# Optimization experiments

Hardware: AMD Instinct MI355X
Metric: run time of the kernel (lower is better)

Reference implementation:

```python
import jax, jax.numpy as jnp
import numpy as np

B, N, D, H, L = 1024, 500, 128, 8, 2  # batch, nb_nodes, dim_emb, nb_heads, nb_layers_decoder
CLIP = 10.0


def _mha(q, K, V, h, mask, clip):
    # q: (B,1,D) single query; K,V: (B,N,D); mask: (B,N) True = forbidden
    Bsz, Nn, Dd = K.shape
    dh = Dd // h
    qh = q.reshape(Bsz, h, dh)            # head k takes contiguous chunk of dim_emb (matches torch view)
    Kh = K.reshape(Bsz, Nn, h, dh)
    Vh = V.reshape(Bsz, Nn, h, dh)
    scores = jnp.einsum('bhd,bnhd->bhn', qh, Kh) / jnp.sqrt(jnp.asarray(dh, q.dtype))
    if clip is not None:
        scores = clip * jnp.tanh(scores)
    scores = jnp.where(mask[:, None, :], jnp.asarray(-1e9, scores.dtype), scores)
    w = jax.nn.softmax(scores, axis=-1)   # (B,h,N)
    out = jnp.einsum('bhn,bnhd->bhd', w, Vh).reshape(Bsz, 1, Dd)
    return out, w.mean(axis=1, keepdims=True)  # (B,1,D), (B,1,N)


def setup_inputs() -> dict:
    key = jax.random.key(0)
    ks = jax.random.split(key, 8)
    query = jax.random.normal(ks[0], (B, 1, D), dtype=jnp.float32)
    K_att = jax.random.normal(ks[1], (B, N, D * L), dtype=jnp.float32)
    V_att = jax.random.normal(ks[2], (B, N, D * L), dtype=jnp.float32)
    mask = jax.random.bernoulli(ks[3], 0.3, (B, N))
    mask = mask.at[:, 0].set(False)  # guarantee every row has a legal action
    s = 1.0 / np.sqrt(D)
    W0_w = jax.random.normal(ks[4], (D, D), dtype=jnp.float32) * s
    W0_b = jnp.zeros((D,), dtype=jnp.float32)
    Wq_w = jax.random.normal(ks[5], (D, D), dtype=jnp.float32) * s
    Wq_b = jnp.zeros((D,), dtype=jnp.float32)
    return {"query": query, "K_att": K_att, "V_att": V_att, "mask": mask,
            "W0_w": W0_w, "W0_b": W0_b, "Wq_w": Wq_w, "Wq_b": Wq_b}


def reference(query, K_att, V_att, mask, W0_w, W0_b, Wq_w, Wq_b):
    q = query
    attn_w = None
    for l in range(L):
        Kl = K_att[:, :, l * D:(l + 1) * D]
        Vl = V_att[:, :, l * D:(l + 1) * D]
        if l < L - 1:
            out, _ = _mha(q, Kl, Vl, H, mask, None)
            q = out @ W0_w.T + W0_b
        else:
            qf = q @ Wq_w.T + Wq_b
            _, attn_w = _mha(qf, Kl, Vl, 1, mask, CLIP)
    return attn_w[:, 0, :]  # (B, N) prob of next node
```

## Files before the change

### kernel.cpp

```cpp
#include <hip/hip_runtime.h>
#include <hip/hip_bf16.h>
#include <math.h>

constexpr int NKEY = 500;
constexpr int DIM = 128;
constexpr int ROWSTRIDE = 256;

typedef __attribute__((ext_vector_type(4))) float f32x4;

__device__ __forceinline__ f32x4 nt_load4(const float* p) {
    return __builtin_nontemporal_load((const f32x4*)p);
}
__device__ __forceinline__ void nt_store(float* p, float v) {
    __builtin_nontemporal_store(v, p);
}

__global__ __launch_bounds__(256, 4)
void fused_pomo_attn(const float* __restrict__ query,
                     const float* __restrict__ K_att,
                     const float* __restrict__ V_att,
                     const int*   __restrict__ mask,
                     const float* __restrict__ W0_w,
                     const float* __restrict__ W0_b,
                     const float* __restrict__ Wq_w,
                     const float* __restrict__ Wq_b,
                     float* __restrict__ out)
{
    const int b = blockIdx.x;
    const int tid = threadIdx.x;
    const int lane32 = tid & 31;
    const int grp = tid >> 5;

    __shared__ alignas(16) float s_red[8][DIM];
    __shared__ float s_m8[8][32];
    __shared__ float s_l8[8][32];
    __shared__ alignas(16) float s_out[DIM];
    __shared__ alignas(16) float s_q1[DIM];
    __shared__ alignas(16) float s_qf[DIM];
    __shared__ alignas(16) float s_s1[NKEY];
    __shared__ int s_idx[NKEY];
    __shared__ int s_cnt;
    __shared__ float s_m[4], s_l[4];

    const size_t brow = (size_t)b * NKEY;

    if (tid < 64) {
        int off = 0;
        for (int base = 0; base < NKEY; base += 64) {
            const int n = base + tid;
            const bool keep = (n < NKEY) && (mask[brow + n] == 0);
            const unsigned long long bal = __ballot(keep);
            const int pre = __popcll(bal & ((1ull << tid) - 1ull));
            if (keep) s_idx[off + pre] = n;
            off += __popcll(bal);
        }
        if (tid == 0) s_cnt = off;
    }
    __syncthreads();
    const int M = s_cnt;
    const int Mm1 = M - 1;

    {
        const f32x4 q4 = ((const f32x4*)(query + (size_t)b * DIM))[lane32];
        const float* Kb = K_att + brow * ROWSTRIDE + lane32 * 4;
        const float* Vb = V_att + brow * ROWSTRIDE + lane32 * 4;
        float m = -1e30f, l = 0.f;
        f32x4 acc; acc[0]=0.f; acc[1]=0.f; acc[2]=0.f; acc[3]=0.f;
        for (int base = 0; base < M; base += 64) {
            int n[8]; bool okv[8];
            #pragma unroll
            for (int j = 0; j < 8; j++) {
                const int p = base + 8*j + grp;
                okv[j] = p < M;
                n[j] = s_idx[okv[j] ? p : Mm1];
            }
            f32x4 k[8], v[8];
            #pragma unroll
            for (int j = 0; j < 8; j++) k[j] = nt_load4(Kb + (size_t)n[j] * ROWSTRIDE);
            #pragma unroll
            for (int j = 0; j < 8; j++) v[j] = nt_load4(Vb + (size_t)n[j] * ROWSTRIDE);
            float s[8];
            #pragma unroll
            for (int j = 0; j < 8; j++)
                s[j] = q4[0]*k[j][0] + q4[1]*k[j][1] + q4[2]*k[j][2] + q4[3]*k[j][3];
            #pragma unroll
            for (int j = 0; j < 8; j++) { s[j] += __shfl_xor(s[j], 1); s[j] += __shfl_xor(s[j], 2); }
            #pragma unroll
            for (int j = 0; j < 8; j++) s[j] = okv[j] ? s[j] * 0.25f : -1e30f;
            float m2 = m;
            #pragma unroll
            for (int j = 0; j < 8; j++) m2 = fmaxf(m2, s[j]);
            const float f = __expf(m - m2);
            float w[8];
            #pragma unroll
            for (int j = 0; j < 8; j++) w[j] = __expf(s[j] - m2);
            l = l * f + ((w[0]+w[1]) + (w[2]+w[3])) + ((w[4]+w[5]) + (w[6]+w[7]));
            #pragma unroll
            for (int d = 0; d < 4; d++) {
                float a = acc[d] * f;
                #pragma unroll
                for (int j = 0; j < 8; j++) a += w[j] * v[j][d];
                acc[d] = a;
            }
            m = m2;
        }
        ((f32x4*)s_red[grp])[lane32] = acc;
        s_m8[grp][lane32] = m;
        s_l8[grp][lane32] = l;
    }
    __syncthreads();
    if (tid < DIM) {
        const int ql = tid >> 2;
        float M_ = -1e30f;
        #pragma unroll
        for (int g = 0; g < 8; g++) M_ = fmaxf(M_, s_m8[g][ql]);
        float L = 0.f, o = 0.f;
        #pragma unroll
        for (int g = 0; g < 8; g++) {
            const float f = __expf(s_m8[g][ql] - M_);
            L += s_l8[g][ql] * f;
            o += s_red[g][tid] * f;
        }
        s_out[tid] = o / L;
    }
    __syncthreads();

    {
        const int i = tid >> 1, half = tid & 1;
        const float4* wrow = (const float4*)(W0_w + (size_t)i * DIM + half * 64);
        float ssum = 0.f;
        #pragma unroll
        for (int k = 0; k < 16; k++) {
            const float4 w4 = wrow[k];
            const float4 o4 = ((const float4*)s_out)[half * 16 + k];
            ssum += w4.x*o4.x + w4.y*o4.y + w4.z*o4.z + w4.w*o4.w;
        }
        ssum += __shfl_xor(ssum, 1);
        if (half == 0) s_q1[i] = ssum + W0_b[i];
    }
    __syncthreads();

    {
        const int i = tid >> 1, half = tid & 1;
        const float4* wrow = (const float4*)(Wq_w + (size_t)i * DIM + half * 64);
        float ssum = 0.f;
        #pragma unroll
        for (int k = 0; k < 16; k++) {
            const float4 w4 = wrow[k];
            const float4 o4 = ((const float4*)s_q1)[half * 16 + k];
            ssum += w4.x*o4.x + w4.y*o4.y + w4.z*o4.z + w4.w*o4.w;
        }
        ssum += __shfl_xor(ssum, 1);
        if (half == 0) s_qf[i] = ssum + Wq_b[i];
    }
    __syncthreads();

    {
        const f32x4 qf4 = ((const f32x4*)s_qf)[lane32];
        const float* K1b = K_att + brow * ROWSTRIDE + DIM + lane32 * 4;
        for (int base = 0; base < M; base += 128) {
            int p[16]; bool ok[16]; int n[16];
            #pragma unroll
            for (int j = 0; j < 16; j++) {
                p[j] = base + 8*j + grp;
                ok[j] = p[j] < M;
                n[j] = s_idx[ok[j] ? p[j] : Mm1];
            }
            f32x4 k[16];
            #pragma unroll
            for (int j = 0; j < 16; j++) k[j] = nt_load4(K1b + (size_t)n[j] * ROWSTRIDE);
            float s[16];
            #pragma unroll
            for (int j = 0; j < 16; j++)
                s[j] = qf4[0]*k[j][0] + qf4[1]*k[j][1] + qf4[2]*k[j][2] + qf4[3]*k[j][3];
            #pragma unroll
            for (int o = 1; o < 32; o <<= 1) {
                #pragma unroll
                for (int j = 0; j < 16; j++) s[j] += __shfl_xor(s[j], o);
            }
            if (lane32 == 0) {
                #pragma unroll
                for (int j = 0; j < 16; j++)
                    if (ok[j]) s_s1[p[j]] = 10.f * tanhf(s[j] * 0.08838834764831845f);
            }
        }
    }
    for (int n = tid; n < NKEY; n += 256) nt_store(out + brow + n, 0.f);
    __syncthreads();

    {
        const int wid = tid >> 6;
        const int lane = tid & 63;
        float m = -INFINITY;
        for (int p = tid; p < M; p += 256) m = fmaxf(m, s_s1[p]);
        #pragma unroll
        for (int o = 32; o > 0; o >>= 1) m = fmaxf(m, __shfl_xor(m, o));
        if (lane == 0) s_m[wid] = m;
        __syncthreads();
        m = fmaxf(fmaxf(s_m[0], s_m[1]), fmaxf(s_m[2], s_m[3]));
        float l = 0.f;
        for (int p = tid; p < M; p += 256) {
            const float e = __expf(s_s1[p] - m);
            s_s1[p] = e;
            l += e;
        }
        #pragma unroll
        for (int o = 32; o > 0; o >>= 1) l += __shfl_xor(l, o);
        if (lane == 0) s_l[wid] = l;
        __syncthreads();
        l = s_l[0] + s_l[1] + s_l[2] + s_l[3];
        const float inv = 1.f / l;
        for (int p = tid; p < M; p += 256) nt_store(out + brow + s_idx[p], s_s1[p] * inv);
    }
}

extern "C" void kernel_launch(void* const* d_in, const int* in_sizes, int n_in,
                              void* d_out, int out_size, void* d_ws, size_t ws_size,
                              hipStream_t stream) {
    const float* query = (const float*)d_in[0];
    const float* K_att = (const float*)d_in[1];
    const float* V_att = (const float*)d_in[2];
    const int*   mask  = (const int*)d_in[3];
    const float* W0_w  = (const float*)d_in[4];
    const float* W0_b  = (const float*)d_in[5];
    const float* Wq_w  = (const float*)d_in[6];
    const float* Wq_b  = (const float*)d_in[7];
    float* out = (float*)d_out;

    const int B = in_sizes[0] / DIM;
    fused_pomo_attn<<<B, 256, 0, stream>>>(query, K_att, V_att, mask,
                                           W0_w, W0_b, Wq_w, Wq_b, out);
}
```

Baseline: 104.8 us.

## Shrink unroll depth, raise occupancy, software-pipeline layer-2 K loads, fast tanh

Cuts the per-iteration gather width in both attention loops from 8/16 rows to 4 rows and raises the launch-bounds occupancy hint from 4 to 5 blocks per SM, to lower register pressure and fit more waves. The second-layer score loop is restructured to prefetch the next chunk of K rows while computing the current one (double buffering). It also replaces tanhf with an exp-based fast tanh. The trade-off is fewer loads in flight per wave in exchange for more resident waves, plus slightly lower tanh accuracy.

```diff
diff --git a/kernel.cpp b/kernel.cpp
--- a/kernel.cpp
+++ b/kernel.cpp
@@ -14,8 +14,14 @@
 __device__ __forceinline__ void nt_store(float* p, float v) {
     __builtin_nontemporal_store(v, p);
 }
-
-__global__ __launch_bounds__(256, 4)
+__device__ __forceinline__ float fast_tanh10(float x) {
+    const float ax = fabsf(x);
+    const float e = __expf(2.f * ax);
+    const float r = 1.f - 2.f / (e + 1.f);
+    return copysignf(10.f * r, x);
+}
+
+__global__ __launch_bounds__(256, 5)
 void fused_pomo_attn(const float* __restrict__ query,
                      const float* __restrict__ K_att,
                      const float* __restrict__ V_att,
@@ -66,40 +72,40 @@
         const float* Vb = V_att + brow * ROWSTRIDE + lane32 * 4;
         float m = -1e30f, l = 0.f;
         f32x4 acc; acc[0]=0.f; acc[1]=0.f; acc[2]=0.f; acc[3]=0.f;
-        for (int base = 0; base < M; base += 64) {
-            int n[8]; bool okv[8];
-            #pragma unroll
-            for (int j = 0; j < 8; j++) {
+        for (int base = 0; base < M; base += 32) {
+            int n[4]; bool okv[4];
+            #pragma unroll
+            for (int j = 0; j < 4; j++) {
                 const int p = base + 8*j + grp;
                 okv[j] = p < M;
                 n[j] = s_idx[okv[j] ? p : Mm1];
             }
-            f32x4 k[8], v[8];
-            #pragma unroll
-            for (int j = 0; j < 8; j++) k[j] = nt_load4(Kb + (size_t)n[j] * ROWSTRIDE);
-            #pragma unroll
-            for (int j = 0; j < 8; j++) v[j] = nt_load4(Vb + (size_t)n[j] * ROWSTRIDE);
-            float s[8];
-            #pragma unroll
-            for (int j = 0; j < 8; j++)
+            f32x4 k[4], v[4];
+            #pragma unroll
+            for (int j = 0; j < 4; j++) k[j] = nt_load4(Kb + (size_t)n[j] * ROWSTRIDE);
+            #pragma unroll
+            for (int j = 0; j < 4; j++) v[j] = nt_load4(Vb + (size_t)n[j] * ROWSTRIDE);
+            float s[4];
+            #pragma unroll
+            for (int j = 0; j < 4; j++)
                 s[j] = q4[0]*k[j][0] + q4[1]*k[j][1] + q4[2]*k[j][2] + q4[3]*k[j][3];
             #pragma unroll
-            for (int j = 0; j < 8; j++) { s[j] += __shfl_xor(s[j], 1); s[j] += __shfl_xor(s[j], 2); }
-            #pragma unroll
-            for (int j = 0; j < 8; j++) s[j] = okv[j] ? s[j] * 0.25f : -1e30f;
+            for (int j = 0; j < 4; j++) { s[j] += __shfl_xor(s[j], 1); s[j] += __shfl_xor(s[j], 2); }
+            #pragma unroll
+            for (int j = 0; j < 4; j++) s[j] = okv[j] ? s[j] * 0.25f : -1e30f;
             float m2 = m;
             #pragma unroll
-            for (int j = 0; j < 8; j++) m2 = fmaxf(m2, s[j]);
+            for (int j = 0; j < 4; j++) m2 = fmaxf(m2, s[j]);
             const float f = __expf(m - m2);
-            float w[8];
-            #pragma unroll
-            for (int j = 0; j < 8; j++) w[j] = __expf(s[j] - m2);
-            l = l * f + ((w[0]+w[1]) + (w[2]+w[3])) + ((w[4]+w[5]) + (w[6]+w[7]));
+            float w[4];
+            #pragma unroll
+            for (int j = 0; j < 4; j++) w[j] = __expf(s[j] - m2);
+            l = l * f + (w[0] + w[1]) + (w[2] + w[3]);
             #pragma unroll
             for (int d = 0; d < 4; d++) {
                 float a = acc[d] * f;
                 #pragma unroll
-                for (int j = 0; j < 8; j++) a += w[j] * v[j][d];
+                for (int j = 0; j < 4; j++) a += w[j] * v[j][d];
                 acc[d] = a;
             }
             m = m2;
@@ -158,31 +164,39 @@
     {
         const f32x4 qf4 = ((const f32x4*)s_qf)[lane32];
         const float* K1b = K_att + brow * ROWSTRIDE + DIM + lane32 * 4;
-        for (int base = 0; base < M; base += 128) {
-            int p[16]; bool ok[16]; int n[16];
-            #pragma unroll
-            for (int j = 0; j < 16; j++) {
-                p[j] = base + 8*j + grp;
-                ok[j] = p[j] < M;
-                n[j] = s_idx[ok[j] ? p[j] : Mm1];
-            }
-            f32x4 k[16];
-            #pragma unroll
-            for (int j = 0; j < 16; j++) k[j] = nt_load4(K1b + (size_t)n[j] * ROWSTRIDE);
-            float s[16];
-            #pragma unroll
-            for (int j = 0; j < 16; j++)
-                s[j] = qf4[0]*k[j][0] + qf4[1]*k[j][1] + qf4[2]*k[j][2] + qf4[3]*k[j][3];
+        f32x4 kt[4];
+        #pragma unroll
+        for (int j = 0; j < 4; j++) {
+            const int p = 8*j + grp;
+            const int nn = s_idx[p < M ? p : Mm1];
+            kt[j] = nt_load4(K1b + (size_t)nn * ROWSTRIDE);
+        }
+        for (int base = 0; base < M; base += 32) {
+            f32x4 kn[4];
+            #pragma unroll
+            for (int j = 0; j < 4; j++) {
+                const int p = base + 32 + 8*j + grp;
+                const int nn = s_idx[p < M ? p : Mm1];
+                kn[j] = nt_load4(K1b + (size_t)nn * ROWSTRIDE);
+            }
+            float s[4];
+            #pragma unroll
+            for (int j = 0; j < 4; j++)
+                s[j] = qf4[0]*kt[j][0] + qf4[1]*kt[j][1] + qf4[2]*kt[j][2] + qf4[3]*kt[j][3];
             #pragma unroll
             for (int o = 1; o < 32; o <<= 1) {
                 #pragma unroll
-                for (int j = 0; j < 16; j++) s[j] += __shfl_xor(s[j], o);
+                for (int j = 0; j < 4; j++) s[j] += __shfl_xor(s[j], o);
             }
             if (lane32 == 0) {
                 #pragma unroll
-                for (int j = 0; j < 16; j++)
-                    if (ok[j]) s_s1[p[j]] = 10.f * tanhf(s[j] * 0.08838834764831845f);
-            }
+                for (int j = 0; j < 4; j++) {
+                    const int p = base + 8*j + grp;
+                    if (p < M) s_s1[p] = fast_tanh10(s[j] * 0.08838834764831845f);
+                }
+            }
+            #pragma unroll
+            for (int j = 0; j < 4; j++) kt[j] = kn[j];
         }
     }
     for (int n = tid; n < NKEY; n += 256) nt_store(out + brow + n, 0.f);
```

New measurement: 104.8 us. Within noise of the previous version (+0.0%).
